# Kernel optimization log

Hardware: AMD Instinct MI355X
Metric: run time of the kernel (lower is better)

## Reference

```python
import jax, jax.numpy as jnp
import numpy as np

U_NUM = 100000
I_NUM = 50000
D = 64
E = 4_000_000
N_LAYERS = 3


def setup_inputs() -> dict:
    key = jax.random.key(0)
    k1, k2, k3, k4 = jax.random.split(key, 4)
    return {
        "user_emb": jax.random.normal(k1, (U_NUM + 1, D), dtype=jnp.float32) * 0.1,
        "item_emb": jax.random.normal(k2, (I_NUM + 1, D), dtype=jnp.float32) * 0.1,
        "edge_user": jax.random.randint(k3, (E,), 0, U_NUM + 1, dtype=jnp.int32),
        "edge_item": jax.random.randint(k4, (E,), 0, I_NUM + 1, dtype=jnp.int32),
    }


def reference(user_emb, item_emb, edge_user, edge_item):
    U = user_emb.shape[0]
    I = item_emb.shape[0]
    N = U + I
    # Symmetrize bipartite interaction edges into full-graph COO indices.
    rows = jnp.concatenate([edge_user, edge_item + U])          # [2E]
    cols = jnp.concatenate([edge_item + U, edge_user])          # [2E]
    # Symmetric degree normalization: A_hat = D^-1/2 A D^-1/2 (deg + 1e-7)
    deg = jax.ops.segment_sum(jnp.ones(rows.shape[0], dtype=jnp.float32), rows, num_segments=N) + 1e-7
    d_inv_sqrt = deg ** -0.5
    vals = d_inv_sqrt[rows] * d_inv_sqrt[cols]                  # [2E]

    emb = jnp.concatenate([user_emb, item_emb], axis=0)         # [N, D]
    acc = emb
    x = emb
    for _ in range(N_LAYERS):
        # SpMM: x_new[r] = sum_{edges (r,c)} vals * x[c]
        x = jax.ops.segment_sum(vals[:, None] * x[cols], rows, num_segments=N)
        acc = acc + x
    total = acc / jnp.float32(N_LAYERS + 1)                     # mean over layer stack
    return total[:U], total[U:]
```

## Files before the change

### kernel.cpp

```cpp
#include <hip/hip_runtime.h>


static constexpr int D = 64;
#define BSHIFT 9
#define BROWS 512
#define KP 512
#define TILE 2048
#define PADSLACK (7 * BROWS)

__device__ __forceinline__ float bflo(unsigned v) {
    unsigned u = v << 16;
    return __builtin_bit_cast(float, u);
}
__device__ __forceinline__ float bfhi(unsigned v) {
    unsigned u = v & 0xFFFF0000u;
    return __builtin_bit_cast(float, u);
}
__device__ __forceinline__ unsigned pack_bf16x2(float a, float b) {
    unsigned ua = __builtin_bit_cast(unsigned, a);
    unsigned ub = __builtin_bit_cast(unsigned, b);
    ua += 0x7FFFu + ((ua >> 16) & 1u);
    ub += 0x7FFFu + ((ub >> 16) & 1u);
    return (ua >> 16) | (ub & 0xFFFF0000u);
}

__global__ __launch_bounds__(256) void bucket_count(
        const int* __restrict__ eu, const int* __restrict__ ei,
        int* __restrict__ bcnt, int E, int U, int twoE) {
    __shared__ int h[KP];
    int tid = threadIdx.x;
    h[tid] = 0; h[tid + 256] = 0;
    __syncthreads();
    for (int e = blockIdx.x * blockDim.x + tid; e < twoE; e += gridDim.x * blockDim.x) {
        int r = (e < E) ? eu[e] : U + ei[e - E];
        atomicAdd(&h[r >> BSHIFT], 1);
    }
    __syncthreads();
    if (h[tid]) atomicAdd(&bcnt[tid], h[tid]);
    if (h[tid + 256]) atomicAdd(&bcnt[tid + 256], h[tid + 256]);
}

__global__ void bscan(const int* __restrict__ bcnt, int* __restrict__ bbase,
                      int* __restrict__ bcursor, int KB, int twoE) {
    __shared__ int s[KP];
    int tid = threadIdx.x;
    int v = (tid < KB) ? bcnt[tid] : 0;
    s[tid] = v;
    __syncthreads();
    for (int off = 1; off < KP; off <<= 1) {
        int a = (tid >= off) ? s[tid - off] : 0;
        __syncthreads();
        s[tid] += a;
        __syncthreads();
    }
    int ex = s[tid] - v;
    if (tid < KB) { bbase[tid] = ex; bcursor[tid] = ex; }
    if (tid == KB) bbase[tid] = twoE;
    if (tid >= KB) bcursor[tid] = 0;
}

__global__ __launch_bounds__(256) void bucket_scatter(
        const int* __restrict__ eu, const int* __restrict__ ei,
        int* __restrict__ bcursor, unsigned* __restrict__ pairs,
        int E, int U, int twoE) {
    __shared__ int hist[KP];
    __shared__ int sbase[KP];
    __shared__ int gbase[KP];
    __shared__ unsigned staging[TILE];
    __shared__ unsigned short sb[TILE];
    int tid = threadIdx.x;
    hist[tid] = 0; hist[tid + 256] = 0;
    __syncthreads();
    int base_e = blockIdx.x * TILE;
    int bk[8]; unsigned pk[8];
#pragma unroll
    for (int k = 0; k < 8; ++k) {
        int e = base_e + k * 256 + tid;
        bk[k] = -1;
        if (e < twoE) {
            int r, c;
            if (e < E) { r = eu[e]; c = U + ei[e]; }
            else       { c = eu[e - E]; r = U + ei[e - E]; }
            int b = r >> BSHIFT;
            bk[k] = b;
            pk[k] = ((unsigned)(r & (BROWS - 1)) << 18) | (unsigned)c;
            atomicAdd(&hist[b], 1);
        }
    }
    __syncthreads();
    int c0 = hist[tid], c1 = hist[tid + 256];
    for (int off = 1; off < KP; off <<= 1) {
        int v0 = (tid >= off) ? hist[tid - off] : 0;
        int v1 = hist[tid + 256 - off];
        __syncthreads();
        hist[tid] += v0; hist[tid + 256] += v1;
        __syncthreads();
    }
    int e0 = hist[tid] - c0, e1 = hist[tid + 256] - c1;
    sbase[tid] = e0; sbase[tid + 256] = e1;
    if (c0 > 0) gbase[tid] = atomicAdd(&bcursor[tid], c0);
    if (c1 > 0) gbase[tid + 256] = atomicAdd(&bcursor[tid + 256], c1);
    hist[tid] = e0; hist[tid + 256] = e1;
    __syncthreads();
#pragma unroll
    for (int k = 0; k < 8; ++k) {
        if (bk[k] >= 0) {
            int pos = atomicAdd(&hist[bk[k]], 1);
            staging[pos] = pk[k];
            sb[pos] = (unsigned short)bk[k];
        }
    }
    __syncthreads();
    int tile_n = min(TILE, twoE - base_e);
#pragma unroll
    for (int k = 0; k < 8; ++k) {
        int j = k * 256 + tid;
        if (j < tile_n) {
            int b = sb[j];
            pairs[gbase[b] + (j - sbase[b])] = staging[j];
        }
    }
}

__global__ __launch_bounds__(512) void csr_build(
        const unsigned* __restrict__ pairs, const int* __restrict__ bbase,
        int* __restrict__ deg, int* __restrict__ row_ptr, float* __restrict__ dis,
        int* __restrict__ cols, int N) {
    __shared__ int cnt[BROWS];
    __shared__ int cur[BROWS];
    __shared__ int fin[BROWS];
    int tid = threadIdx.x;
    int b = blockIdx.x;
    int lo = bbase[b], hi = bbase[b + 1];
    int cbase = lo + PADSLACK * b;
    cnt[tid] = 0;
    __syncthreads();
    for (int i = lo + tid; i < hi; i += 512) atomicAdd(&cnt[pairs[i] >> 18], 1);
    __syncthreads();
    int c = cnt[tid];
    int p = (c + 7) & ~7;
    cnt[tid] = p;
    __syncthreads();
    for (int off = 1; off < BROWS; off <<= 1) {
        int a = (tid >= off) ? cnt[tid - off] : 0;
        __syncthreads();
        cnt[tid] += a;
        __syncthreads();
    }
    int e = cnt[tid] - p;
    int r = (b << BSHIFT) + tid;
    if (r < N) {
        deg[r] = c;
        row_ptr[r] = cbase + e;
        dis[r] = rsqrtf((float)c + 1e-7f);
    }
    cur[tid] = e;
    fin[tid] = e + p;
    __syncthreads();
    for (int i = lo + tid; i < hi; i += 512) {
        unsigned pe = pairs[i];
        int pos = atomicAdd(&cur[pe >> 18], 1);
        cols[cbase + pos] = (int)(pe & 0x3FFFFu);
    }
    __syncthreads();
    for (int i = cur[tid]; i < fin[tid]; ++i) cols[cbase + i] = N;
}

__global__ void init_kernel(const float* __restrict__ ue, const float* __restrict__ ie,
                            const float* __restrict__ dis, unsigned* __restrict__ xs,
                            float2* __restrict__ acc2, int UD2, int ND2) {
    int t = blockIdx.x * blockDim.x + threadIdx.x;
    if (t >= ND2 + 32) return;
    if (t >= ND2) { xs[t] = 0u; return; }
    const float* src = (t < UD2) ? ue : ie;
    int tt = (t < UD2) ? t : t - UD2;
    float v0 = src[2 * tt];
    float v1 = src[2 * tt + 1];
    acc2[t] = make_float2(v0, v1);
    float dv = dis[t >> 5];
    xs[t] = pack_bf16x2(dv * v0, dv * v1);
}

__global__ __launch_bounds__(256) void spmm_kernel(
        const int* __restrict__ row_ptr, const int* __restrict__ deg,
        const float* __restrict__ dis, const int* __restrict__ cols,
        const unsigned* __restrict__ xs, unsigned* __restrict__ xs_next,
        float4* __restrict__ acc4, int N, float final_scale) {
    int wid = blockIdx.x * 4 + (threadIdx.x >> 6);
    if (wid >= N) return;
    int lane = threadIdx.x & 63;
    int n8 = lane >> 3;
    int dp = lane & 7;
    int start = row_ptr[wid];
    int cntp = (deg[wid] + 7) & ~7;
    float dr = dis[wid];
    const int* colp = cols + start;
    int vbase = n8 << 2;
    int dpo = dp << 2;
    float s0 = 0.f, s1 = 0.f, s2 = 0.f, s3 = 0.f;
    float s4 = 0.f, s5 = 0.f, s6 = 0.f, s7 = 0.f;
    for (int chunk = 0; chunk < cntp; chunk += 64) {
        int cv = colp[chunk + lane];
        int nq = min(64, cntp - chunk) >> 3;
        for (int q = 0; q < nq; ++q) {
            int co = __builtin_amdgcn_ds_bpermute((q << 5) + vbase, cv);
            const uint4* p = (const uint4*)(xs + (((unsigned)co) << 5) + dpo);
            uint4 v = *p;
            s0 += bflo(v.x); s1 += bfhi(v.x);
            s2 += bflo(v.y); s3 += bfhi(v.y);
            s4 += bflo(v.z); s5 += bfhi(v.z);
            s6 += bflo(v.w); s7 += bfhi(v.w);
        }
    }
#pragma unroll
    for (int m = 8; m < 64; m <<= 1) {
        s0 += __shfl_xor(s0, m); s1 += __shfl_xor(s1, m);
        s2 += __shfl_xor(s2, m); s3 += __shfl_xor(s3, m);
        s4 += __shfl_xor(s4, m); s5 += __shfl_xor(s5, m);
        s6 += __shfl_xor(s6, m); s7 += __shfl_xor(s7, m);
    }
    if (n8 == 0) {
        float x0 = dr * s0, x1 = dr * s1, x2 = dr * s2, x3 = dr * s3;
        float x4 = dr * s4, x5 = dr * s5, x6 = dr * s6, x7 = dr * s7;
        uint4 w;
        w.x = pack_bf16x2(dr * x0, dr * x1);
        w.y = pack_bf16x2(dr * x2, dr * x3);
        w.z = pack_bf16x2(dr * x4, dr * x5);
        w.w = pack_bf16x2(dr * x6, dr * x7);
        ((uint4*)xs_next)[(wid << 3) + dp] = w;
        int o = (wid << 4) + (dp << 1);
        float4 a = acc4[o];
        a.x = (a.x + x0) * final_scale;
        a.y = (a.y + x1) * final_scale;
        a.z = (a.z + x2) * final_scale;
        a.w = (a.w + x3) * final_scale;
        acc4[o] = a;
        float4 b2 = acc4[o + 1];
        b2.x = (b2.x + x4) * final_scale;
        b2.y = (b2.y + x5) * final_scale;
        b2.z = (b2.z + x6) * final_scale;
        b2.w = (b2.w + x7) * final_scale;
        acc4[o + 1] = b2;
    }
}

extern "C" void kernel_launch(void* const* d_in, const int* in_sizes, int n_in,
                              void* d_out, int out_size, void* d_ws, size_t ws_size,
                              hipStream_t stream) {
    const float* ue = (const float*)d_in[0];
    const float* ie = (const float*)d_in[1];
    const int* eu = (const int*)d_in[2];
    const int* ei = (const int*)d_in[3];
    const int U = in_sizes[0] / D;
    const int I = in_sizes[1] / D;
    const int N = U + I;
    const int E = in_sizes[2];
    const int twoE = 2 * E;
    const int KB = (N + BROWS - 1) / BROWS;
    float* out = (float*)d_out;

    char* ws = (char*)d_ws;
    auto alloc = [&](size_t bytes) {
        char* p = ws;
        ws += (bytes + 255) & ~(size_t)255;
        return p;
    };
    int* deg = (int*)alloc((size_t)N * 4);
    int* row_ptr = (int*)alloc((size_t)N * 4);
    float* dis = (float*)alloc((size_t)N * 4);
    int* bcnt = (int*)alloc(KP * 4);
    int* bbase = (int*)alloc((KP + 1) * 4);
    int* bcursor = (int*)alloc(KP * 4);
    int* cols = (int*)alloc(((size_t)twoE + (size_t)PADSLACK * (KB + 1) + 256) * 4);
    unsigned* pairs = (unsigned*)alloc((size_t)twoE * 4);
    unsigned* xsA = (unsigned*)alloc(((size_t)N + 1) * 32 * 4);
    unsigned* xsB = (unsigned*)alloc(((size_t)N + 1) * 32 * 4);

    hipMemsetAsync(bcnt, 0, KP * 4, stream);
    bucket_count<<<1024, 256, 0, stream>>>(eu, ei, bcnt, E, U, twoE);
    bscan<<<1, KP, 0, stream>>>(bcnt, bbase, bcursor, KB, twoE);
    bucket_scatter<<<(twoE + TILE - 1) / TILE, 256, 0, stream>>>(
        eu, ei, bcursor, pairs, E, U, twoE);
    csr_build<<<KB, 512, 0, stream>>>(pairs, bbase, deg, row_ptr, dis, cols, N);

    int ND2 = N * 32, UD2 = U * 32;
    init_kernel<<<(ND2 + 32 + 255) / 256, 256, 0, stream>>>(
        ue, ie, dis, xsA, (float2*)out, UD2, ND2);

    unsigned* x = xsA;
    unsigned* xn = xsB;
    for (int l = 0; l < 3; ++l) {
        float fs = (l == 2) ? 0.25f : 1.0f;
        spmm_kernel<<<(N + 3) / 4, 256, 0, stream>>>(
            row_ptr, deg, dis, cols, x, xn, (float4*)out, N, fs);
        unsigned* tmp = x; x = xn; xn = tmp;
    }
}
```

Measured before the change: 683.5 us.

## Compute degrees in bucket_count, shrink CSR buckets, vectorize init

Degree counting moves into bucket_count through global atomics, so csr_build no longer makes a separate histogram pass over the pairs. Buckets shrink to 256 rows, giving 1024 buckets and twice as many csr_build blocks of 256 threads each. init_kernel now computes the inverse sqrt degree itself and uses float4/uint4 vector loads and stores. The cost is 8M global atomics on deg, and the padding slack (7×BROWS per bucket) is halved.

Result: slower. 953.9 us (+39.6%).

```diff
diff --git a/kernel.cpp b/kernel.cpp
--- a/kernel.cpp
+++ b/kernel.cpp
@@ -2,9 +2,9 @@
 
 
 static constexpr int D = 64;
-#define BSHIFT 9
-#define BROWS 512
-#define KP 512
+#define BSHIFT 8
+#define BROWS 256
+#define KP 1024
 #define TILE 2048
 #define PADSLACK (7 * BROWS)
 
@@ -26,18 +26,26 @@
 
 __global__ __launch_bounds__(256) void bucket_count(
         const int* __restrict__ eu, const int* __restrict__ ei,
-        int* __restrict__ bcnt, int E, int U, int twoE) {
+        int* __restrict__ bcnt, int* __restrict__ deg, int E, int U) {
     __shared__ int h[KP];
     int tid = threadIdx.x;
-    h[tid] = 0; h[tid + 256] = 0;
-    __syncthreads();
-    for (int e = blockIdx.x * blockDim.x + tid; e < twoE; e += gridDim.x * blockDim.x) {
-        int r = (e < E) ? eu[e] : U + ei[e - E];
-        atomicAdd(&h[r >> BSHIFT], 1);
-    }
-    __syncthreads();
-    if (h[tid]) atomicAdd(&bcnt[tid], h[tid]);
-    if (h[tid + 256]) atomicAdd(&bcnt[tid + 256], h[tid + 256]);
+#pragma unroll
+    for (int k = 0; k < 4; ++k) h[tid + k * 256] = 0;
+    __syncthreads();
+    for (int e = blockIdx.x * blockDim.x + tid; e < E; e += gridDim.x * blockDim.x) {
+        int u = eu[e];
+        int it = U + ei[e];
+        atomicAdd(&h[u >> BSHIFT], 1);
+        atomicAdd(&h[it >> BSHIFT], 1);
+        atomicAdd(&deg[u], 1);
+        atomicAdd(&deg[it], 1);
+    }
+    __syncthreads();
+#pragma unroll
+    for (int k = 0; k < 4; ++k) {
+        int v = h[tid + k * 256];
+        if (v) atomicAdd(&bcnt[tid + k * 256], v);
+    }
 }
 
 __global__ void bscan(const int* __restrict__ bcnt, int* __restrict__ bbase,
@@ -56,7 +64,7 @@
     int ex = s[tid] - v;
     if (tid < KB) { bbase[tid] = ex; bcursor[tid] = ex; }
     if (tid == KB) bbase[tid] = twoE;
-    if (tid >= KB) bcursor[tid] = 0;
+    if (tid > KB) bcursor[tid] = 0;
 }
 
 __global__ __launch_bounds__(256) void bucket_scatter(
@@ -69,7 +77,8 @@
     __shared__ unsigned staging[TILE];
     __shared__ unsigned short sb[TILE];
     int tid = threadIdx.x;
-    hist[tid] = 0; hist[tid + 256] = 0;
+#pragma unroll
+    for (int k = 0; k < 4; ++k) hist[tid + k * 256] = 0;
     __syncthreads();
     int base_e = blockIdx.x * TILE;
     int bk[8]; unsigned pk[8];
@@ -88,19 +97,29 @@
         }
     }
     __syncthreads();
-    int c0 = hist[tid], c1 = hist[tid + 256];
+    int cc[4];
+#pragma unroll
+    for (int k = 0; k < 4; ++k) cc[k] = hist[tid + k * 256];
     for (int off = 1; off < KP; off <<= 1) {
-        int v0 = (tid >= off) ? hist[tid - off] : 0;
-        int v1 = hist[tid + 256 - off];
-        __syncthreads();
-        hist[tid] += v0; hist[tid + 256] += v1;
-        __syncthreads();
-    }
-    int e0 = hist[tid] - c0, e1 = hist[tid + 256] - c1;
-    sbase[tid] = e0; sbase[tid + 256] = e1;
-    if (c0 > 0) gbase[tid] = atomicAdd(&bcursor[tid], c0);
-    if (c1 > 0) gbase[tid + 256] = atomicAdd(&bcursor[tid + 256], c1);
-    hist[tid] = e0; hist[tid + 256] = e1;
+        int a[4];
+#pragma unroll
+        for (int k = 0; k < 4; ++k) {
+            int idx = tid + k * 256;
+            a[k] = (idx >= off) ? hist[idx - off] : 0;
+        }
+        __syncthreads();
+#pragma unroll
+        for (int k = 0; k < 4; ++k) hist[tid + k * 256] += a[k];
+        __syncthreads();
+    }
+#pragma unroll
+    for (int k = 0; k < 4; ++k) {
+        int idx = tid + k * 256;
+        int e0 = hist[idx] - cc[k];
+        sbase[idx] = e0;
+        if (cc[k] > 0) gbase[idx] = atomicAdd(&bcursor[idx], cc[k]);
+        hist[idx] = e0;
+    }
     __syncthreads();
 #pragma unroll
     for (int k = 0; k < 8; ++k) {
@@ -122,42 +141,34 @@
     }
 }
 
-__global__ __launch_bounds__(512) void csr_build(
+__global__ __launch_bounds__(256) void csr_build(
         const unsigned* __restrict__ pairs, const int* __restrict__ bbase,
-        int* __restrict__ deg, int* __restrict__ row_ptr, float* __restrict__ dis,
+        const int* __restrict__ deg, int* __restrict__ row_ptr,
         int* __restrict__ cols, int N) {
-    __shared__ int cnt[BROWS];
+    __shared__ int sc[BROWS];
     __shared__ int cur[BROWS];
     __shared__ int fin[BROWS];
     int tid = threadIdx.x;
     int b = blockIdx.x;
     int lo = bbase[b], hi = bbase[b + 1];
     int cbase = lo + PADSLACK * b;
-    cnt[tid] = 0;
-    __syncthreads();
-    for (int i = lo + tid; i < hi; i += 512) atomicAdd(&cnt[pairs[i] >> 18], 1);
-    __syncthreads();
-    int c = cnt[tid];
+    int r = (b << BSHIFT) + tid;
+    int c = (r < N) ? deg[r] : 0;
     int p = (c + 7) & ~7;
-    cnt[tid] = p;
+    sc[tid] = p;
     __syncthreads();
     for (int off = 1; off < BROWS; off <<= 1) {
-        int a = (tid >= off) ? cnt[tid - off] : 0;
-        __syncthreads();
-        cnt[tid] += a;
-        __syncthreads();
-    }
-    int e = cnt[tid] - p;
-    int r = (b << BSHIFT) + tid;
-    if (r < N) {
-        deg[r] = c;
-        row_ptr[r] = cbase + e;
-        dis[r] = rsqrtf((float)c + 1e-7f);
-    }
+        int a = (tid >= off) ? sc[tid - off] : 0;
+        __syncthreads();
+        sc[tid] += a;
+        __syncthreads();
+    }
+    int e = sc[tid] - p;
+    if (r < N) row_ptr[r] = cbase + e;
     cur[tid] = e;
     fin[tid] = e + p;
     __syncthreads();
-    for (int i = lo + tid; i < hi; i += 512) {
+    for (int i = lo + tid; i < hi; i += 256) {
         unsigned pe = pairs[i];
         int pos = atomicAdd(&cur[pe >> 18], 1);
         cols[cbase + pos] = (int)(pe & 0x3FFFFu);
@@ -166,19 +177,33 @@
     for (int i = cur[tid]; i < fin[tid]; ++i) cols[cbase + i] = N;
 }
 
-__global__ void init_kernel(const float* __restrict__ ue, const float* __restrict__ ie,
-                            const float* __restrict__ dis, unsigned* __restrict__ xs,
-                            float2* __restrict__ acc2, int UD2, int ND2) {
+__global__ __launch_bounds__(256) void init_kernel(
+        const float4* __restrict__ ue4, const float4* __restrict__ ie4,
+        const int* __restrict__ deg, float* __restrict__ dis,
+        uint4* __restrict__ xsA4, uint4* __restrict__ xsB4,
+        float4* __restrict__ acc4, int U8, int N8) {
     int t = blockIdx.x * blockDim.x + threadIdx.x;
-    if (t >= ND2 + 32) return;
-    if (t >= ND2) { xs[t] = 0u; return; }
-    const float* src = (t < UD2) ? ue : ie;
-    int tt = (t < UD2) ? t : t - UD2;
-    float v0 = src[2 * tt];
-    float v1 = src[2 * tt + 1];
-    acc2[t] = make_float2(v0, v1);
-    float dv = dis[t >> 5];
-    xs[t] = pack_bf16x2(dv * v0, dv * v1);
+    if (t >= N8 + 8) return;
+    if (t >= N8) {
+        uint4 z = {0u, 0u, 0u, 0u};
+        xsA4[t] = z;
+        xsB4[t] = z;
+        return;
+    }
+    int row = t >> 3;
+    float dv = rsqrtf((float)deg[row] + 1e-7f);
+    if ((t & 7) == 0) dis[row] = dv;
+    const float4* src = (t < U8) ? (ue4 + 2 * t) : (ie4 + 2 * (t - U8));
+    float4 a0 = src[0];
+    float4 a1 = src[1];
+    acc4[2 * t] = a0;
+    acc4[2 * t + 1] = a1;
+    uint4 w;
+    w.x = pack_bf16x2(dv * a0.x, dv * a0.y);
+    w.y = pack_bf16x2(dv * a0.z, dv * a0.w);
+    w.z = pack_bf16x2(dv * a1.x, dv * a1.y);
+    w.w = pack_bf16x2(dv * a1.z, dv * a1.w);
+    xsA4[t] = w;
 }
 
 __global__ __launch_bounds__(256) void spmm_kernel(
@@ -266,9 +291,9 @@
         return p;
     };
     int* deg = (int*)alloc((size_t)N * 4);
+    int* bcnt = (int*)alloc(KP * 4);
     int* row_ptr = (int*)alloc((size_t)N * 4);
     float* dis = (float*)alloc((size_t)N * 4);
-    int* bcnt = (int*)alloc(KP * 4);
     int* bbase = (int*)alloc((KP + 1) * 4);
     int* bcursor = (int*)alloc(KP * 4);
     int* cols = (int*)alloc(((size_t)twoE + (size_t)PADSLACK * (KB + 1) + 256) * 4);
@@ -276,16 +301,18 @@
     unsigned* xsA = (unsigned*)alloc(((size_t)N + 1) * 32 * 4);
     unsigned* xsB = (unsigned*)alloc(((size_t)N + 1) * 32 * 4);
 
-    hipMemsetAsync(bcnt, 0, KP * 4, stream);
-    bucket_count<<<1024, 256, 0, stream>>>(eu, ei, bcnt, E, U, twoE);
+    size_t z0 = (((size_t)N * 4 + 255) & ~(size_t)255) + KP * 4;
+    hipMemsetAsync(deg, 0, z0, stream);
+    bucket_count<<<1024, 256, 0, stream>>>(eu, ei, bcnt, deg, E, U);
     bscan<<<1, KP, 0, stream>>>(bcnt, bbase, bcursor, KB, twoE);
     bucket_scatter<<<(twoE + TILE - 1) / TILE, 256, 0, stream>>>(
         eu, ei, bcursor, pairs, E, U, twoE);
-    csr_build<<<KB, 512, 0, stream>>>(pairs, bbase, deg, row_ptr, dis, cols, N);
-
-    int ND2 = N * 32, UD2 = U * 32;
-    init_kernel<<<(ND2 + 32 + 255) / 256, 256, 0, stream>>>(
-        ue, ie, dis, xsA, (float2*)out, UD2, ND2);
+    csr_build<<<KB, BROWS, 0, stream>>>(pairs, bbase, deg, row_ptr, cols, N);
+
+    int N8 = N * 8, U8 = U * 8;
+    init_kernel<<<(N8 + 8 + 255) / 256, 256, 0, stream>>>(
+        (const float4*)ue, (const float4*)ie, deg, dis,
+        (uint4*)xsA, (uint4*)xsB, (float4*)out, U8, N8);
 
     unsigned* x = xsA;
     unsigned* xn = xsB;
```
